# Optimization experiments

Hardware: AMD Instinct MI355X
Metric: run time of the kernel (lower is better)

## Reference

```python
import jax, jax.numpy as jnp
import numpy as np

B, IMG, TXT, DIM, H, D = 1, 1024, 256, 1536, 24, 64
SCALE = 1.0  # control cross-attn scale


def _lin(x, w, b):
    return x @ w + b


def _heads(x):  # [B,S,DIM] -> [B,H,S,D]
    return jnp.swapaxes(x.reshape(x.shape[0], x.shape[1], H, D), 1, 2)


def _merge(x):  # [B,H,S,D] -> [B,S,DIM]
    return jnp.swapaxes(x, 1, 2).reshape(x.shape[0], x.shape[2], H * D)


def _sdpa(q, k, v):
    s = jnp.einsum('bhqd,bhkd->bhqk', q, k) * (1.0 / np.sqrt(D))
    return jnp.einsum('bhqk,bhkd->bhqd', jax.nn.softmax(s, axis=-1), v)


def _rope(x, pe):  # x: [B,H,S,D], pe: [1,1,S,D//2,2,2]
    xr = x.reshape(*x.shape[:-1], -1, 1, 2)  # [B,H,S,D/2,1,2]
    out = pe[..., 0] * xr[..., 0] + pe[..., 1] * xr[..., 1]  # [B,H,S,D/2,2]
    return out.reshape(x.shape)


def _forward(hidden_states, encoder_hidden_states, hidden_states_control,
             encoder_hidden_states_control, img_to_q_control, pe,
             a_q_w, a_q_b, a_k_w, a_k_b, a_v_w, a_v_b,
             a_addq_w, a_addq_b, a_addk_w, a_addk_b, a_addv_w, a_addv_b,
             a_out_w, a_out_b, a_addout_w, a_addout_b,
             c_q_w, c_q_b, c_k_w, c_k_b, c_v_w, c_v_b,
             c_addq_w, c_addq_b, c_addk_w, c_addk_b, c_addv_w, c_addv_b,
             c_out_w, c_out_b, c_addout_w, c_addout_b):
    img_len = hidden_states.shape[1]
    # ---- main joint attention stream (no RoPE, per original) ----
    q = jnp.concatenate([_heads(_lin(hidden_states, a_q_w, a_q_b)),
                         _heads(_lin(encoder_hidden_states, a_addq_w, a_addq_b))], axis=2)
    k = jnp.concatenate([_heads(_lin(hidden_states, a_k_w, a_k_b)),
                         _heads(_lin(encoder_hidden_states, a_addk_w, a_addk_b))], axis=2)
    v = jnp.concatenate([_heads(_lin(hidden_states, a_v_w, a_v_b)),
                         _heads(_lin(encoder_hidden_states, a_addv_w, a_addv_b))], axis=2)
    hs = _merge(_sdpa(q, k, v))
    hs, ehs = hs[:, :img_len], hs[:, img_len:]
    # ---- control joint attention stream (with RoPE) ----
    qc = jnp.concatenate([_heads(_lin(hidden_states_control, c_q_w, c_q_b)),
                          _heads(_lin(encoder_hidden_states_control, c_addq_w, c_addq_b))], axis=2)
    kc = jnp.concatenate([_heads(_lin(hidden_states_control, c_k_w, c_k_b)),
                          _heads(_lin(encoder_hidden_states_control, c_addk_w, c_addk_b))], axis=2)
    vc = jnp.concatenate([_heads(_lin(hidden_states_control, c_v_w, c_v_b)),
                          _heads(_lin(encoder_hidden_states_control, c_addv_w, c_addv_b))], axis=2)
    key_cross, value_cross = kc, vc  # saved BEFORE RoPE, per original
    hsc = _merge(_sdpa(_rope(qc, pe), _rope(kc, pe), vc))
    hsc, ehsc = hsc[:, :img_len], hsc[:, img_len:]
    # ---- cross attention: img query attends to control K/V ----
    q_cross = _rope(_heads(img_to_q_control), pe[:, :, :img_len])
    k_cross = _rope(key_cross, pe[:, :, :key_cross.shape[2]])
    cross = _merge(_sdpa(q_cross, k_cross, value_cross))
    hs = hs + SCALE * cross
    # ---- output projections (to_out[1] is dropout p=0 -> identity) ----
    hs = _lin(hs, a_out_w, a_out_b)
    ehs = _lin(ehs, a_addout_w, a_addout_b)
    hsc = _lin(hsc, c_out_w, c_out_b)
    ehsc = _lin(ehsc, c_addout_w, c_addout_b)
    return hs, ehs, hsc, ehsc


def setup_inputs() -> dict:
    key = jax.random.key(0)
    ki = iter(jax.random.split(key, 80))
    d = {}
    d['hidden_states'] = jax.random.normal(next(ki), (B, IMG, DIM), jnp.float32)
    d['encoder_hidden_states'] = jax.random.normal(next(ki), (B, TXT, DIM), jnp.float32)
    d['hidden_states_control'] = jax.random.normal(next(ki), (B, IMG, DIM), jnp.float32)
    d['encoder_hidden_states_control'] = jax.random.normal(next(ki), (B, TXT, DIM), jnp.float32)
    d['img_to_q_control'] = jax.random.normal(next(ki), (B, IMG, DIM), jnp.float32)
    # realistic rotary pe: [1,1,S,D/2,2,2] rotation matrices
    S = IMG + TXT
    pos = np.arange(S, dtype=np.float32)
    freqs = 1.0 / (10000.0 ** (np.arange(0, D, 2, dtype=np.float32) / D))  # [D/2]
    ang = pos[:, None] * freqs[None, :]  # [S, D/2]
    cos, sin = np.cos(ang), np.sin(ang)
    pe = np.stack([np.stack([cos, -sin], -1), np.stack([sin, cos], -1)], -2)  # [S,D/2,2,2]
    d['pe'] = jnp.asarray(pe)[None, None]
    for p in ('a', 'c'):
        for name in ('q', 'k', 'v', 'addq', 'addk', 'addv', 'out', 'addout'):
            d[f'{p}_{name}_w'] = jax.random.normal(next(ki), (DIM, DIM), jnp.float32) * 0.02
            d[f'{p}_{name}_b'] = jax.random.normal(next(ki), (DIM,), jnp.float32) * 0.01
    return d


def reference(hidden_states, encoder_hidden_states, hidden_states_control,
              encoder_hidden_states_control, img_to_q_control, pe,
              a_q_w, a_q_b, a_k_w, a_k_b, a_v_w, a_v_b,
              a_addq_w, a_addq_b, a_addk_w, a_addk_b, a_addv_w, a_addv_b,
              a_out_w, a_out_b, a_addout_w, a_addout_b,
              c_q_w, c_q_b, c_k_w, c_k_b, c_v_w, c_v_b,
              c_addq_w, c_addq_b, c_addk_w, c_addk_b, c_addv_w, c_addv_b,
              c_out_w, c_out_b, c_addout_w, c_addout_b):
    return _forward(hidden_states, encoder_hidden_states, hidden_states_control,
                    encoder_hidden_states_control, img_to_q_control, pe,
                    a_q_w, a_q_b, a_k_w, a_k_b, a_v_w, a_v_b,
                    a_addq_w, a_addq_b, a_addk_w, a_addk_b, a_addv_w, a_addv_b,
                    a_out_w, a_out_b, a_addout_w, a_addout_b,
                    c_q_w, c_q_b, c_k_w, c_k_b, c_v_w, c_v_b,
                    c_addq_w, c_addq_b, c_addk_w, c_addk_b, c_addv_w, c_addv_b,
                    c_out_w, c_out_b, c_addout_w, c_addout_b)
```

## Files before the change

kernel.cpp:

```cpp
#include <hip/hip_runtime.h>

#define DIM 1536
#define IMG 1024
#define TXT 256
#define SEQ 1280
#define NH 24
#define HD 64
#define SD ((size_t)SEQ * DIM)
#define IDSZ ((size_t)IMG * DIM)
#define WSZ ((size_t)DIM * DIM)

typedef __attribute__((ext_vector_type(8))) short short8;
typedef __attribute__((ext_vector_type(4))) float f32x4;

__device__ __forceinline__ float bf2f(ushort u) {
    union { unsigned int i; float f; } v; v.i = ((unsigned int)u) << 16; return v.f;
}
__device__ __forceinline__ ushort f2bf(float f) {
    union { unsigned int i; float f; } v; v.f = f;
    unsigned int u = v.i;
    u += 0x7fffu + ((u >> 16) & 1u);
    return (ushort)(u >> 16);
}
__device__ __forceinline__ ushort f2bf_rz(float f) {
    union { unsigned int i; float f; } v; v.f = f;
    return (ushort)(v.i >> 16);
}

__global__ __launch_bounds__(256) void detect_dtype(const void* __restrict__ p,
                                                    int* __restrict__ flag)
{
    __shared__ int cnt;
    if (threadIdx.x == 0) cnt = 0;
    __syncthreads();
    const ushort* u = (const ushort*)p;
    int local = 0;
    for (int i = threadIdx.x; i < 2048; i += 256) {
        ushort v = u[2 * i];
        int e = (v >> 7) & 0xFF;
        if (e >= 0xC0) local++;
    }
    atomicAdd(&cnt, local);
    __syncthreads();
    if (threadIdx.x == 0) flag[0] = (cnt > 16) ? 1 : 0;
}

struct CvtP {
    const void* src[20];
    ushort* dst[20];
    int n8[20];
};

__global__ __launch_bounds__(256) void convert_bf16(CvtP p, const int* __restrict__ dflag)
{
    const int a = blockIdx.y;
    const int i = blockIdx.x * 256 + threadIdx.x;
    if (i >= p.n8[a]) return;
    const size_t off = (size_t)i * 8;
    uint4 o;
    if (dflag[0]) {
        const float* s = (const float*)p.src[a] + off;
        const float4 f0 = *(const float4*)s;
        const float4 f1 = *(const float4*)(s + 4);
        ushort t[8];
        t[0] = f2bf(f0.x); t[1] = f2bf(f0.y); t[2] = f2bf(f0.z); t[3] = f2bf(f0.w);
        t[4] = f2bf(f1.x); t[5] = f2bf(f1.y); t[6] = f2bf(f1.z); t[7] = f2bf(f1.w);
        o = *(uint4*)t;
    } else {
        o = *(const uint4*)((const ushort*)p.src[a] + off);
    }
    *(uint4*)(p.dst[a] + off) = o;
}

#define LSTR 40

struct QKV3P {
    const ushort* Xb;
    const ushort* Wb;
    const void* B[12];
    float* Y[6];
    ushort* Yh[6];
    ushort* Yl[6];
};

__global__ __launch_bounds__(256) void gemm_qkv_v4(QKV3P p, const int* __restrict__ dflag)
{
    __shared__ __align__(16) ushort As[2][128 * LSTR];
    __shared__ __align__(16) ushort Bs[2][64 * 64];
    const int dt = dflag[0];
    const int bx = blockIdx.x;
    const int wsel = bx / 12;
    const int n0 = (bx - wsel * 12) * 128;
    const int ys = blockIdx.y;
    const int str = (ys >= 10) ? 1 : 0;
    const int m0g = (ys - str * 10) * 128;
    const bool istxt = (m0g >= IMG);
    const int widx = str * 6 + wsel + (istxt ? 3 : 0);
    const ushort* X  = p.Xb + (size_t)str * SD;
    const ushort* Wp = p.Wb + (size_t)widx * WSZ;
    const void* Bp = p.B[widx];
    const int yidx = str * 3 + wsel;
    float*  Y  = p.Y[yidx];
    ushort* yh = p.Yh[yidx];
    ushort* yl = p.Yl[yidx];

    const int t = threadIdx.x;
    const int wave = t >> 6, lane = t & 63;
    const int quad = lane >> 4, l16 = lane & 15;
    const int wm = (wave >> 1) * 64, wn = (wave & 1) * 64;

    const int arow = t >> 1, apair = t & 1;
    const int bn8 = (t & 15) << 3, bkk = (t >> 4) << 1;
    const int aps = apair ^ ((arow >> 3) & 1);
    const int adst = arow * LSTR + aps * 16;
    const int bkg = bkk >> 3, bo = bkk & 7;

    f32x4 acc[4][4];
#pragma unroll
    for (int i = 0; i < 4; ++i)
#pragma unroll
        for (int j = 0; j < 4; ++j) acc[i][j] = (f32x4)(0.0f);

    uint4 rau[2];
    uint4 rbu[2];

    auto loadA = [&](int k0) {
        const ushort* xp = X + (size_t)(m0g + arow) * DIM + k0 + apair * 16;
        rau[0] = *(const uint4*)xp;
        rau[1] = *(const uint4*)(xp + 8);
    };
    auto loadB = [&](int k0) {
        const ushort* wp0 = Wp + (size_t)(k0 + bkk) * DIM + n0 + bn8;
        rbu[0] = *(const uint4*)wp0;
        rbu[1] = *(const uint4*)(wp0 + DIM);
    };
    auto storeA = [&](int buf) {
        *(uint4*)&As[buf][adst]     = rau[0];
        *(uint4*)&As[buf][adst + 8] = rau[1];
    };
    auto storeB = [&](int buf) {
        ushort t0[8], t1[8];
        *(uint4*)t0 = rbu[0];
        *(uint4*)t1 = rbu[1];
#pragma unroll
        for (int j = 0; j < 8; ++j) {
            const int rr = bn8 + j;
            const int R = rr & 63, half = rr >> 6;
            const int gx = (((half << 2) + bkg) ^ (R & 7) ^ (R >> 3)) & 7;
            *(unsigned int*)&Bs[buf][R * 64 + gx * 8 + bo] =
                (unsigned int)t0[j] | ((unsigned int)t1[j] << 16);
        }
    };

    loadA(0); loadB(0);
    storeA(0); storeB(0);
    __syncthreads();

    for (int k = 0; k < DIM / 32; ++k) {
        const int cur = k & 1;
        const bool hn = (k + 1) < DIM / 32;
        if (hn) { loadA((k + 1) * 32); loadB((k + 1) * 32); }

        short8 b[4];
#pragma unroll
        for (int j = 0; j < 4; ++j) {
            const int rrn = wn + j * 16 + l16;
            const int R = rrn & 63, half = rrn >> 6;
            const int gx = (((half << 2) + quad) ^ (R & 7) ^ (R >> 3)) & 7;
            b[j] = *(const short8*)&Bs[cur][R * 64 + gx * 8];
        }
#pragma unroll
        for (int i = 0; i < 4; ++i) {
            const int rr = wm + i * 16 + l16;
            const int ps = (quad >> 1) ^ ((rr >> 3) & 1);
            const int col = ps * 16 + (quad & 1) * 8;
            short8 a = *(const short8*)&As[cur][rr * LSTR + col];
#pragma unroll
            for (int j = 0; j < 4; ++j)
                acc[i][j] = __builtin_amdgcn_mfma_f32_16x16x32_bf16(a, b[j], acc[i][j], 0, 0, 0);
        }
        if (hn) { storeA(cur ^ 1); storeB(cur ^ 1); }
        __syncthreads();
    }

#pragma unroll
    for (int j = 0; j < 4; ++j) {
        const int col = n0 + wn + j * 16 + l16;
        const float bv = dt ? ((const float*)Bp)[col] : bf2f(((const ushort*)Bp)[col]);
#pragma unroll
        for (int i = 0; i < 4; ++i)
#pragma unroll
            for (int r = 0; r < 4; ++r) {
                const int row = m0g + wm + i * 16 + quad * 4 + r;
                const size_t o = (size_t)row * DIM + col;
                const float val = acc[i][j][r] + bv;
                if (Y) Y[o] = val;
                if (yh) {
                    const ushort hv = f2bf(val);
                    yh[o] = hv;
                    yl[o] = f2bf(val - bf2f(hv));
                }
            }
    }
}

struct OutP {
    const ushort* Xh; const ushort* Xl;
    const ushort* Wb;
    const void* B[4];
    void* out;
};

__global__ __launch_bounds__(256) void gemm_out_v4(OutP p, const int* __restrict__ dflag)
{
    __shared__ __align__(16) ushort Ah[2][64 * LSTR];
    __shared__ __align__(16) ushort Al[2][64 * LSTR];
    __shared__ __align__(16) ushort Bs[2][64 * 64];
    const int dt = dflag[0];
    const int n0 = blockIdx.x * 128;
    const int mt = blockIdx.y;
    const int seg = (mt < 16) ? 0 : (mt < 20) ? 1 : (mt < 36) ? 2 : 3;
    const ushort* Wp = p.Wb + (size_t)seg * WSZ;
    const void* Bp = p.B[seg];
    const int m0 = mt * 64;

    const int t = threadIdx.x;
    const int wave = t >> 6, lane = t & 63;
    const int quad = lane >> 4, l16 = lane & 15;
    const int wm = (wave >> 1) * 32, wn = (wave & 1) * 64;

    const int arow = t >> 2, ag = t & 3;
    const int apg = ag >> 1, asub = ag & 1;
    const int aps = apg ^ ((arow >> 3) & 1);
    const int adst = arow * LSTR + aps * 16 + asub * 8;
    const int bn8 = (t & 15) << 3, bkk = (t >> 4) << 1;
    const int bkg = bkk >> 3, bo = bkk & 7;

    f32x4 acc[2][4];
#pragma unroll
    for (int i = 0; i < 2; ++i)
#pragma unroll
        for (int j = 0; j < 4; ++j) acc[i][j] = (f32x4)(0.0f);

    uint4 rah, ral;
    uint4 rbu[2];

    auto loadA = [&](int k0) {
        const size_t off = (size_t)(m0 + arow) * DIM + k0 + ag * 8;
        rah = *(const uint4*)(p.Xh + off);
        ral = *(const uint4*)(p.Xl + off);
    };
    auto loadB = [&](int k0) {
        const ushort* wp0 = Wp + (size_t)(k0 + bkk) * DIM + n0 + bn8;
        rbu[0] = *(const uint4*)wp0;
        rbu[1] = *(const uint4*)(wp0 + DIM);
    };
    auto storeA = [&](int buf) {
        *(uint4*)&Ah[buf][adst] = rah;
        *(uint4*)&Al[buf][adst] = ral;
    };
    auto storeB = [&](int buf) {
        ushort t0[8], t1[8];
        *(uint4*)t0 = rbu[0];
        *(uint4*)t1 = rbu[1];
#pragma unroll
        for (int j = 0; j < 8; ++j) {
            const int rr = bn8 + j;
            const int R = rr & 63, half = rr >> 6;
            const int gx = (((half << 2) + bkg) ^ (R & 7) ^ (R >> 3)) & 7;
            *(unsigned int*)&Bs[buf][R * 64 + gx * 8 + bo] =
                (unsigned int)t0[j] | ((unsigned int)t1[j] << 16);
        }
    };

    loadA(0); loadB(0);
    storeA(0); storeB(0);
    __syncthreads();

    for (int k = 0; k < DIM / 32; ++k) {
        const int cur = k & 1;
        const bool hn = (k + 1) < DIM / 32;
        if (hn) { loadA((k + 1) * 32); loadB((k + 1) * 32); }

        short8 b[4];
#pragma unroll
        for (int j = 0; j < 4; ++j) {
            const int rrn = wn + j * 16 + l16;
            const int R = rrn & 63, half = rrn >> 6;
            const int gx = (((half << 2) + quad) ^ (R & 7) ^ (R >> 3)) & 7;
            b[j] = *(const short8*)&Bs[cur][R * 64 + gx * 8];
        }
#pragma unroll
        for (int i = 0; i < 2; ++i) {
            const int rr = wm + i * 16 + l16;
            const int ps = (quad >> 1) ^ ((rr >> 3) & 1);
            const int col = ps * 16 + (quad & 1) * 8;
            short8 ah = *(const short8*)&Ah[cur][rr * LSTR + col];
            short8 al = *(const short8*)&Al[cur][rr * LSTR + col];
#pragma unroll
            for (int j = 0; j < 4; ++j) {
                acc[i][j] = __builtin_amdgcn_mfma_f32_16x16x32_bf16(ah, b[j], acc[i][j], 0, 0, 0);
                acc[i][j] = __builtin_amdgcn_mfma_f32_16x16x32_bf16(al, b[j], acc[i][j], 0, 0, 0);
            }
        }
        if (hn) { storeA(cur ^ 1); storeB(cur ^ 1); }
        __syncthreads();
    }

#pragma unroll
    for (int j = 0; j < 4; ++j) {
        const int col = n0 + wn + j * 16 + l16;
        const float bv = dt ? ((const float*)Bp)[col] : bf2f(((const ushort*)Bp)[col]);
#pragma unroll
        for (int i = 0; i < 2; ++i)
#pragma unroll
            for (int r = 0; r < 4; ++r) {
                const int grow = m0 + wm + i * 16 + quad * 4 + r;
                const size_t o = (size_t)grow * DIM + col;
                const float val = acc[i][j][r] + bv;
                if (dt) ((float*)p.out)[o] = val;
                else    ((ushort*)p.out)[o] = f2bf(val);
            }
    }
}

__device__ __forceinline__ void pe_load(const void* pe, int dt, size_t off,
                                        float& c00, float& c01, float& c10, float& c11)
{
    if (dt) {
        float4 pv = *(const float4*)((const float*)pe + off);
        c00 = pv.x; c01 = pv.y; c10 = pv.z; c11 = pv.w;
    } else {
        const ushort* pp = (const ushort*)pe + off;
        c00 = bf2f(pp[0]); c01 = bf2f(pp[1]); c10 = bf2f(pp[2]); c11 = bf2f(pp[3]);
    }
}

struct PrepP {
    const float* v1; const float* vC;
    ushort *vthA, *vtlA, *vthC, *vtlC;
    float* q1;
    const float* k1; ushort *khC, *kloC;
    const void* i2q; float* qx;
    const void* pe;
};

#define VT_BLKS 960
#define RN0 (SEQ * 768)
#define RN1 (SEQ * 768)
#define RN2 (IMG * 768)

__global__ __launch_bounds__(256) void prep_fused(PrepP p, const int* __restrict__ dflag)
{
    __shared__ unsigned int tile[64 * 65];
    const int dt = dflag[0];
    const int bx = blockIdx.x;
    const int t = threadIdx.x;

    if (bx < VT_BLKS) {
        const int z = bx / 480, rem = bx - z * 480;
        const int s0 = (rem % 20) * 64, h = rem / 20;
        const float* V = z ? p.vC : p.v1;
        ushort* Vth = z ? p.vthC : p.vthA;
        ushort* Vtl = z ? p.vtlC : p.vtlA;
#pragma unroll
        for (int it = 0; it < 16; ++it) {
            const int sl = (t >> 6) + (it << 2);
            const int d = t & 63;
            const float v = V[(size_t)(s0 + sl) * DIM + h * HD + d];
            const ushort hv = f2bf(v);
            const ushort lv = f2bf(v - bf2f(hv));
            tile[d * 65 + sl] = (unsigned int)hv | ((unsigned int)lv << 16);
        }
        __syncthreads();
        const int d = t >> 2, cc = (t & 3) << 4;
        ushort th[16], tl[16];
#pragma unroll
        for (int j = 0; j < 16; ++j) {
            const unsigned int w = tile[d * 65 + cc + j];
            th[j] = (ushort)w;
            tl[j] = (ushort)(w >> 16);
        }
        const size_t off = (size_t)(h * HD + d) * SEQ + s0 + cc;
        *(uint4*)(Vth + off)     = *(uint4*)&th[0];
        *(uint4*)(Vth + off + 8) = *(uint4*)&th[8];
        *(uint4*)(Vtl + off)     = *(uint4*)&tl[0];
        *(uint4*)(Vtl + off + 8) = *(uint4*)&tl[8];
        return;
    }

    int idx = (bx - VT_BLKS) * 256 + t;
    if (idx < RN0) {
        int s = idx / 768, pp = idx - s * 768;
        int col = pp << 1, i = pp & 31;
        float* bp = p.q1 + (size_t)s * DIM + col;
        float x0 = bp[0], x1 = bp[1];
        float c00, c01, c10, c11;
        pe_load(p.pe, dt, (size_t)s * 128 + i * 4, c00, c01, c10, c11);
        bp[0] = c00 * x0 + c01 * x1;
        bp[1] = c10 * x0 + c11 * x1;
        return;
    }
    idx -= RN0;
    if (idx < RN1) {
        int s = idx / 768, pp = idx - s * 768;
        int col = pp << 1, i = pp & 31;
        float2 xv = *(const float2*)(p.k1 + (size_t)s * DIM + col);
        float c00, c01, c10, c11;
        pe_load(p.pe, dt, (size_t)s * 128 + i * 4, c00, c01, c10, c11);
        float y0 = c00 * xv.x + c01 * xv.y;
        float y1 = c10 * xv.x + c11 * xv.y;
        ushort h0 = f2bf(y0), h1 = f2bf(y1);
        ushort l0 = f2bf(y0 - bf2f(h0)), l1 = f2bf(y1 - bf2f(h1));
        *(unsigned int*)(p.khC  + (size_t)s * DIM + col) = (unsigned int)h0 | ((unsigned int)h1 << 16);
        *(unsigned int*)(p.kloC + (size_t)s * DIM + col) = (unsigned int)l0 | ((unsigned int)l1 << 16);
        return;
    }
    idx -= RN1;
    if (idx < RN2) {
        int s = idx / 768, pp = idx - s * 768;
        int col = pp << 1, i = pp & 31;
        float x0, x1;
        if (dt) {
            float2 xv = *(const float2*)((const float*)p.i2q + (size_t)s * DIM + col);
            x0 = xv.x; x1 = xv.y;
        } else {
            const ushort* sp = (const ushort*)p.i2q + (size_t)s * DIM + col;
            x0 = bf2f(sp[0]); x1 = bf2f(sp[1]);
        }
        float c00, c01, c10, c11;
        pe_load(p.pe, dt, (size_t)s * 128 + i * 4, c00, c01, c10, c11);
        float* dp = p.qx + (size_t)s * DIM + col;
        dp[0] = c00 * x0 + c01 * x1;
        dp[1] = c10 * x0 + c11 * x1;
    }
}

__device__ __forceinline__ int swz(int row, int col) {
    return row * 64 + ((((col >> 3) ^ row) & 7) << 3) + (col & 7);
}
__device__ __forceinline__ short8 ldfrag(const ushort* plane, int row, int col) {
    return *(const short8*)&plane[swz(row, col)];
}

struct AttnAllP {
    const float* Qf[3];
    const ushort* Kh[3]; const ushort* Kl[3];
    const ushort* Vth[3]; const ushort* Vtl[3];
    float* Op0[3]; float* Op1[3];
    float2* Ml[3];
    int mlq[3];
};

__global__ __launch_bounds__(256) void attn_all(AttnAllP p)
{
    __shared__ ushort Qh_[4096], Ql_[4096];
    __shared__ ushort Kh_[4096], Kl_[4096];
    __shared__ ushort Vh_[4096], Vl_[4096];

    const int bx = blockIdx.x;
    const int seg = (bx < 20) ? 0 : (bx < 40) ? 1 : 2;
    const int q0 = (bx - ((seg == 0) ? 0 : (seg == 1) ? 20 : 40)) * 64;
    const int h = blockIdx.y;
    const int z = blockIdx.z;
    const int t = threadIdx.x;
    const int wave = t >> 6, lane = t & 63;
    const int quad = lane >> 4, l16 = lane & 15;
    const int wq0 = wave * 16;

    const float* Qf = p.Qf[seg];
    const ushort* Kh = p.Kh[seg]; const ushort* Kl = p.Kl[seg];
    const ushort* Vth = p.Vth[seg]; const ushort* Vtl = p.Vtl[seg];

    const int srow = t >> 2, c0 = (t & 3) << 4;
    const int g0 = c0 >> 3;
    const int p0 = ((g0 ^ (srow & 7)) & 7) << 3;
    const int p1 = (((g0 + 1) ^ (srow & 7)) & 7) << 3;

    {
        const float* src = Qf + (size_t)(q0 + srow) * DIM + h * HD + c0;
        float x[16];
        *(float4*)&x[0]  = *(const float4*)(src);
        *(float4*)&x[4]  = *(const float4*)(src + 4);
        *(float4*)&x[8]  = *(const float4*)(src + 8);
        *(float4*)&x[12] = *(const float4*)(src + 12);
        ushort hi[16], lo[16];
#pragma unroll
        for (int i = 0; i < 16; ++i) {
            const float xs = x[i] * 0.125f;
            hi[i] = f2bf(xs);
            lo[i] = f2bf(xs - bf2f(hi[i]));
        }
        *(uint4*)&Qh_[srow * 64 + p0] = *(uint4*)&hi[0];
        *(uint4*)&Qh_[srow * 64 + p1] = *(uint4*)&hi[8];
        *(uint4*)&Ql_[srow * 64 + p0] = *(uint4*)&lo[0];
        *(uint4*)&Ql_[srow * 64 + p1] = *(uint4*)&lo[8];
    }
    short8 qfh[2], qfl[2];
#pragma unroll
    for (int c = 0; c < 2; ++c) {
        qfh[c] = ldfrag(Qh_, wq0 + l16, c * 32 + quad * 8);
        qfl[c] = ldfrag(Ql_, wq0 + l16, c * 32 + quad * 8);
    }

    float m_[4], l_[4];
#pragma unroll
    for (int r = 0; r < 4; ++r) { m_[r] = -3e38f; l_[r] = 0.0f; }
    f32x4 Oacc[4];
#pragma unroll
    for (int j = 0; j < 4; ++j) Oacc[j] = (f32x4)(0.0f);

    const int kvbeg = z * (SEQ / 2);
    for (int kt = 0; kt < SEQ / 2; kt += 64) {
        const int kv0 = kvbeg + kt;
        __syncthreads();
        {
            const size_t off = (size_t)(kv0 + srow) * DIM + h * HD + c0;
            *(uint4*)&Kh_[srow * 64 + p0] = *(const uint4*)(Kh + off);
            *(uint4*)&Kh_[srow * 64 + p1] = *(const uint4*)(Kh + off + 8);
            *(uint4*)&Kl_[srow * 64 + p0] = *(const uint4*)(Kl + off);
            *(uint4*)&Kl_[srow * 64 + p1] = *(const uint4*)(Kl + off + 8);
        }
        {
            const size_t off = (size_t)(h * HD + srow) * SEQ + kv0 + c0;
            *(uint4*)&Vh_[srow * 64 + p0] = *(const uint4*)(Vth + off);
            *(uint4*)&Vh_[srow * 64 + p1] = *(const uint4*)(Vth + off + 8);
            *(uint4*)&Vl_[srow * 64 + p0] = *(const uint4*)(Vtl + off);
            *(uint4*)&Vl_[srow * 64 + p1] = *(const uint4*)(Vtl + off + 8);
        }
        __syncthreads();

        f32x4 S[4];
#pragma unroll
        for (int j = 0; j < 4; ++j) S[j] = (f32x4)(0.0f);
        __builtin_amdgcn_s_setprio(1);
#pragma unroll
        for (int c = 0; c < 2; ++c) {
#pragma unroll
            for (int j = 0; j < 4; ++j) {
                short8 bh = ldfrag(Kh_, j * 16 + l16, c * 32 + quad * 8);
                short8 bl = ldfrag(Kl_, j * 16 + l16, c * 32 + quad * 8);
                S[j] = __builtin_amdgcn_mfma_f32_16x16x32_bf16(qfh[c], bh, S[j], 0, 0, 0);
                S[j] = __builtin_amdgcn_mfma_f32_16x16x32_bf16(qfl[c], bh, S[j], 0, 0, 0);
                S[j] = __builtin_amdgcn_mfma_f32_16x16x32_bf16(qfh[c], bl, S[j], 0, 0, 0);
            }
        }
        __builtin_amdgcn_s_setprio(0);

        float alpha[4];
#pragma unroll
        for (int r = 0; r < 4; ++r) {
            float mx = fmaxf(fmaxf(S[0][r], S[1][r]), fmaxf(S[2][r], S[3][r]));
            mx = fmaxf(mx, __shfl_xor(mx, 1));
            mx = fmaxf(mx, __shfl_xor(mx, 2));
            mx = fmaxf(mx, __shfl_xor(mx, 4));
            mx = fmaxf(mx, __shfl_xor(mx, 8));
            float mn = fmaxf(m_[r], mx);
            alpha[r] = __expf(m_[r] - mn);
            m_[r] = mn;
            float rs = 0.0f;
#pragma unroll
            for (int j = 0; j < 4; ++j) {
                float pv = __expf(S[j][r] - mn);
                S[j][r] = pv;
                rs += pv;
            }
            rs += __shfl_xor(rs, 1);
            rs += __shfl_xor(rs, 2);
            rs += __shfl_xor(rs, 4);
            rs += __shfl_xor(rs, 8);
            l_[r] = l_[r] * alpha[r] + rs;
        }
#pragma unroll
        for (int j = 0; j < 4; ++j)
#pragma unroll
            for (int r = 0; r < 4; ++r) Oacc[j][r] *= alpha[r];

        {
            const int prow = wq0 + quad * 4;
#pragma unroll
            for (int j = 0; j < 4; ++j)
#pragma unroll
                for (int r = 0; r < 4; ++r) {
                    float pv = S[j][r];
                    ushort ph = f2bf(pv);
                    ushort pl = f2bf_rz(pv - bf2f(ph));
                    int idx = swz(prow + r, j * 16 + l16);
                    Qh_[idx] = ph;
                    Ql_[idx] = pl;
                }
        }

        __builtin_amdgcn_s_setprio(1);
#pragma unroll
        for (int c = 0; c < 2; ++c) {
            short8 pah = ldfrag(Qh_, wq0 + l16, c * 32 + quad * 8);
            short8 pal = ldfrag(Ql_, wq0 + l16, c * 32 + quad * 8);
#pragma unroll
            for (int jn = 0; jn < 4; ++jn) {
                short8 vbh = ldfrag(Vh_, jn * 16 + l16, c * 32 + quad * 8);
                short8 vbl = ldfrag(Vl_, jn * 16 + l16, c * 32 + quad * 8);
                Oacc[jn] = __builtin_amdgcn_mfma_f32_16x16x32_bf16(pah, vbh, Oacc[jn], 0, 0, 0);
                Oacc[jn] = __builtin_amdgcn_mfma_f32_16x16x32_bf16(pal, vbh, Oacc[jn], 0, 0, 0);
                Oacc[jn] = __builtin_amdgcn_mfma_f32_16x16x32_bf16(pah, vbl, Oacc[jn], 0, 0, 0);
            }
        }
        __builtin_amdgcn_s_setprio(0);
    }

    float* Opz = z ? p.Op1[seg] : p.Op0[seg];
    const int mlq = p.mlq[seg];
    float2* Ml = p.Ml[seg];
#pragma unroll
    for (int r = 0; r < 4; ++r) {
        const int rowq = q0 + wq0 + quad * 4 + r;
        if (l16 == 0)
            Ml[((size_t)z * NH + h) * mlq + rowq] = make_float2(m_[r], l_[r]);
#pragma unroll
        for (int jn = 0; jn < 4; ++jn)
            Opz[(size_t)rowq * DIM + h * HD + jn * 16 + l16] = Oacc[jn][r];
    }
}

struct MergeP {
    const float *pA0, *pA1, *pC0, *pC1, *pX0, *pX1;
    const float2 *MlA, *MlC, *MlX;
    ushort *Xh, *Xl;
};

__device__ __forceinline__ float4 comb2(const float* O0, const float* O1,
                                        const float2* Ml, int mlq, int row, int c4)
{
    const int h = c4 >> 6;
    const float2 a = Ml[(size_t)h * mlq + row];
    const float2 b = Ml[(size_t)(NH + h) * mlq + row];
    const float ms = fmaxf(a.x, b.x);
    const float s0 = __expf(a.x - ms), s1 = __expf(b.x - ms);
    const float inv = 1.0f / (s0 * a.y + s1 * b.y);
    const float4 o0 = *(const float4*)&O0[(size_t)row * DIM + c4];
    const float4 o1 = *(const float4*)&O1[(size_t)row * DIM + c4];
    float4 r;
    r.x = (s0 * o0.x + s1 * o1.x) * inv;
    r.y = (s0 * o0.y + s1 * o1.y) * inv;
    r.z = (s0 * o0.z + s1 * o1.z) * inv;
    r.w = (s0 * o0.w + s1 * o1.w) * inv;
    return r;
}

__global__ __launch_bounds__(256) void merge_all(MergeP p)
{
    const int idx = blockIdx.x * 256 + threadIdx.x;
    if (idx >= 2560 * 384) return;
    const int row = idx / 384;
    const int c4 = (idx - row * 384) << 2;
    float4 r;
    if (row < SEQ) {
        r = comb2(p.pA0, p.pA1, p.MlA, SEQ, row, c4);
        if (row < IMG) {
            const float4 x = comb2(p.pX0, p.pX1, p.MlX, IMG, row, c4);
            r.x += x.x; r.y += x.y; r.z += x.z; r.w += x.w;
        }
    } else {
        r = comb2(p.pC0, p.pC1, p.MlC, SEQ, row - SEQ, c4);
    }
    float v[4] = {r.x, r.y, r.z, r.w};
    ushort hi[4], lo[4];
#pragma unroll
    for (int j = 0; j < 4; ++j) {
        hi[j] = f2bf(v[j]);
        lo[j] = f2bf(v[j] - bf2f(hi[j]));
    }
    const size_t o = (size_t)row * DIM + c4;
    *(uint2*)(p.Xh + o) = *(uint2*)hi;
    *(uint2*)(p.Xl + o) = *(uint2*)lo;
}

extern "C" void kernel_launch(void* const* d_in, const int* in_sizes, int n_in,
                              void* d_out, int out_size, void* d_ws, size_t ws_size,
                              hipStream_t stream) {
    (void)in_sizes; (void)n_in; (void)out_size; (void)ws_size;
    const void* hs   = d_in[0];
    const void* ehs  = d_in[1];
    const void* hsc  = d_in[2];
    const void* ehsc = d_in[3];
    const void* i2q  = d_in[4];
    const void* pe   = d_in[5];
#define W_(i) ((const void*)d_in[i])

    char* base = (char*)d_ws;
    int* flag = (int*)base;
    char* ptr = base + 256;
    auto alloc = [&](size_t bytes) { char* r = ptr; ptr += bytes; return r; };
    float* q1  = (float*)alloc(SD * 4);
    float* k1  = (float*)alloc(SD * 4);
    float* v1  = (float*)alloc(SD * 4);
    float* vC  = (float*)alloc(SD * 4);
    float* qA  = (float*)alloc(SD * 4);
    float* qx  = (float*)alloc(IDSZ * 4);
    ushort* khA  = (ushort*)alloc(SD * 2);
    ushort* kloA = (ushort*)alloc(SD * 2);
    ushort* vthA = (ushort*)alloc(SD * 2);
    ushort* vtlA = (ushort*)alloc(SD * 2);
    ushort* khC  = (ushort*)alloc(SD * 2);
    ushort* kloC = (ushort*)alloc(SD * 2);
    ushort* vthC = (ushort*)alloc(SD * 2);
    ushort* vtlC = (ushort*)alloc(SD * 2);
    float* pX0 = (float*)alloc(IDSZ * 4);
    float* pX1 = (float*)alloc(IDSZ * 4);
    float2* MlA = (float2*)alloc((size_t)2 * NH * SEQ * 8);
    float2* MlC = (float2*)alloc((size_t)2 * NH * SEQ * 8);
    float2* MlX = (float2*)alloc((size_t)2 * NH * IMG * 8);
    ushort* Wbf = (ushort*)alloc(16 * WSZ * 2);
    ushort* Xbf = (ushort*)alloc(2 * SD * 2);
    float* pC1 = (float*)Xbf;
    ushort* Xh = (ushort*)qA;
    ushort* Xl = (ushort*)q1;

    dim3 blk(256);
    detect_dtype<<<1, blk, 0, stream>>>(hs, flag);

    {
        CvtP cp;
        const int wsrc[16] = {6, 8, 10, 12, 14, 16, 22, 24, 26, 28, 30, 32,
                              18, 20, 34, 36};
        for (int j = 0; j < 16; ++j) {
            cp.src[j] = W_(wsrc[j]);
            cp.dst[j] = Wbf + (size_t)j * WSZ;
            cp.n8[j] = (int)(WSZ / 8);
        }
        cp.src[16] = hs;   cp.dst[16] = Xbf;             cp.n8[16] = (int)(IDSZ / 8);
        cp.src[17] = ehs;  cp.dst[17] = Xbf + IDSZ;      cp.n8[17] = (int)((size_t)TXT * DIM / 8);
        cp.src[18] = hsc;  cp.dst[18] = Xbf + SD;        cp.n8[18] = (int)(IDSZ / 8);
        cp.src[19] = ehsc; cp.dst[19] = Xbf + SD + IDSZ; cp.n8[19] = (int)((size_t)TXT * DIM / 8);
        convert_bf16<<<dim3((int)(WSZ / 8 + 255) / 256, 20), blk, 0, stream>>>(cp, flag);
    }

    QKV3P qp;
    qp.Xb = Xbf;
    qp.Wb = Wbf;
    {
        const int bsrc[12] = {7, 9, 11, 13, 15, 17, 23, 25, 27, 29, 31, 33};
        for (int j = 0; j < 12; ++j) qp.B[j] = W_(bsrc[j]);
    }
    for (int j = 0; j < 6; ++j) { qp.Y[j] = nullptr; qp.Yh[j] = nullptr; qp.Yl[j] = nullptr; }
    qp.Y[0] = qA;
    qp.Yh[1] = khA; qp.Yl[1] = kloA;
    qp.Y[2] = v1;
    qp.Y[3] = q1;
    qp.Y[4] = k1;
    qp.Y[5] = vC;
    gemm_qkv_v4<<<dim3(36, 20), blk, 0, stream>>>(qp, flag);

    {
        PrepP pp;
        pp.v1 = v1; pp.vC = vC;
        pp.vthA = vthA; pp.vtlA = vtlA; pp.vthC = vthC; pp.vtlC = vtlC;
        pp.q1 = q1;
        pp.k1 = k1; pp.khC = khC; pp.kloC = kloC;
        pp.i2q = i2q; pp.qx = qx;
        pp.pe = pe;
        const int ropeBlocks = (RN0 + RN1 + RN2 + 255) / 256;
        prep_fused<<<VT_BLKS + ropeBlocks, blk, 0, stream>>>(pp, flag);
    }

    {
        AttnAllP ap;
        ap.Qf[0] = qA; ap.Qf[1] = q1; ap.Qf[2] = qx;
        ap.Kh[0] = khA; ap.Kl[0] = kloA;
        ap.Kh[1] = khC; ap.Kl[1] = kloC;
        ap.Kh[2] = khC; ap.Kl[2] = kloC;
        ap.Vth[0] = vthA; ap.Vtl[0] = vtlA;
        ap.Vth[1] = vthC; ap.Vtl[1] = vtlC;
        ap.Vth[2] = vthC; ap.Vtl[2] = vtlC;
        ap.Op0[0] = v1;  ap.Op1[0] = k1;
        ap.Op0[1] = vC;  ap.Op1[1] = pC1;
        ap.Op0[2] = pX0; ap.Op1[2] = pX1;
        ap.Ml[0] = MlA; ap.Ml[1] = MlC; ap.Ml[2] = MlX;
        ap.mlq[0] = SEQ; ap.mlq[1] = SEQ; ap.mlq[2] = IMG;
        attn_all<<<dim3(56, NH, 2), blk, 0, stream>>>(ap);
    }

    {
        MergeP mp;
        mp.pA0 = v1; mp.pA1 = k1;
        mp.pC0 = vC; mp.pC1 = pC1;
        mp.pX0 = pX0; mp.pX1 = pX1;
        mp.MlA = MlA; mp.MlC = MlC; mp.MlX = MlX;
        mp.Xh = Xh; mp.Xl = Xl;
        merge_all<<<(2560 * 384 + 255) / 256, blk, 0, stream>>>(mp);
    }

    {
        OutP op;
        op.Xh = Xh; op.Xl = Xl;
        op.Wb = Wbf + (size_t)12 * WSZ;
        op.B[0] = W_(19); op.B[1] = W_(21); op.B[2] = W_(35); op.B[3] = W_(37);
        op.out = d_out;
        gemm_out_v4<<<dim3(12, 40), blk, 0, stream>>>(op, flag);
    }
#undef W_
}
```

Baseline: 552.2 us.

## Pre-swizzle weights into tiled LDS image and drop Q shared buffers in attention

Weight conversion now writes each 32x128 weight tile already laid out in the swizzled LDS format. The QKV and output GEMMs can then load B tiles with contiguous 16-byte loads and store them to LDS with two vector stores, instead of eight scattered 32-bit stores per thread. Separately, the attention kernel reuses the K shared buffers for Q and P staging, which removes the Qh/Ql arrays to cut LDS use and may raise occupancy. This adds a __syncthreads before P is written. The weight conversion kernel is split from the activation conversion.

```diff
diff --git a/kernel.cpp b/kernel.cpp
--- a/kernel.cpp
+++ b/kernel.cpp
@@ -9,6 +9,9 @@
 #define SD ((size_t)SEQ * DIM)
 #define IDSZ ((size_t)IMG * DIM)
 #define WSZ ((size_t)DIM * DIM)
+#define NTIL 12
+#define KTIL 48
+#define TILE_USH 4096
 
 typedef __attribute__((ext_vector_type(8))) short short8;
 typedef __attribute__((ext_vector_type(4))) float f32x4;
@@ -46,9 +49,9 @@
 }
 
 struct CvtP {
-    const void* src[20];
-    ushort* dst[20];
-    int n8[20];
+    const void* src[4];
+    ushort* dst[4];
+    int n8[4];
 };
 
 __global__ __launch_bounds__(256) void convert_bf16(CvtP p, const int* __restrict__ dflag)
@@ -72,32 +75,76 @@
     *(uint4*)(p.dst[a] + off) = o;
 }
 
+struct WImgP {
+    const void* src[16];
+    ushort* img;
+};
+
+__global__ __launch_bounds__(256) void convert_wimg(WImgP p, const int* __restrict__ dflag)
+{
+    const int widx = blockIdx.y;
+    const int nt = blockIdx.x / KTIL, kt = blockIdx.x - nt * KTIL;
+    const int t = threadIdx.x;
+    const int bn8 = (t & 15) << 3, bkk = (t >> 4) << 1;
+    const int bkg = bkk >> 3, bo = bkk & 7;
+    const int k0 = kt * 32, n0 = nt * 128;
+
+    ushort t0[8], t1[8];
+    if (dflag[0]) {
+        const float* w = (const float*)p.src[widx];
+        const float* r0 = w + (size_t)(k0 + bkk) * DIM + n0 + bn8;
+        float x0[8], x1[8];
+        *(float4*)&x0[0] = *(const float4*)r0;
+        *(float4*)&x0[4] = *(const float4*)(r0 + 4);
+        *(float4*)&x1[0] = *(const float4*)(r0 + DIM);
+        *(float4*)&x1[4] = *(const float4*)(r0 + DIM + 4);
+#pragma unroll
+        for (int j = 0; j < 8; ++j) { t0[j] = f2bf(x0[j]); t1[j] = f2bf(x1[j]); }
+    } else {
+        const ushort* w = (const ushort*)p.src[widx];
+        const ushort* r0 = w + (size_t)(k0 + bkk) * DIM + n0 + bn8;
+        *(uint4*)t0 = *(const uint4*)r0;
+        *(uint4*)t1 = *(const uint4*)(r0 + DIM);
+    }
+
+    ushort* img = p.img + (((size_t)widx * NTIL + nt) * KTIL + kt) * TILE_USH;
+#pragma unroll
+    for (int j = 0; j < 8; ++j) {
+        const int rr = bn8 + j;
+        const int R = rr & 63, half = rr >> 6;
+        const int gx = (((half << 2) + bkg) ^ (R & 7) ^ (R >> 3)) & 7;
+        *(unsigned int*)&img[R * 64 + gx * 8 + bo] =
+            (unsigned int)t0[j] | ((unsigned int)t1[j] << 16);
+    }
+}
+
 #define LSTR 40
 
 struct QKV3P {
     const ushort* Xb;
-    const ushort* Wb;
+    const ushort* Wimg;
     const void* B[12];
     float* Y[6];
     ushort* Yh[6];
     ushort* Yl[6];
 };
 
-__global__ __launch_bounds__(256) void gemm_qkv_v4(QKV3P p, const int* __restrict__ dflag)
+__global__ __launch_bounds__(256) void gemm_qkv_v5(QKV3P p, const int* __restrict__ dflag)
 {
     __shared__ __align__(16) ushort As[2][128 * LSTR];
     __shared__ __align__(16) ushort Bs[2][64 * 64];
     const int dt = dflag[0];
     const int bx = blockIdx.x;
     const int wsel = bx / 12;
-    const int n0 = (bx - wsel * 12) * 128;
+    const int nt = bx - wsel * 12;
+    const int n0 = nt * 128;
     const int ys = blockIdx.y;
     const int str = (ys >= 10) ? 1 : 0;
     const int m0g = (ys - str * 10) * 128;
     const bool istxt = (m0g >= IMG);
     const int widx = str * 6 + wsel + (istxt ? 3 : 0);
     const ushort* X  = p.Xb + (size_t)str * SD;
-    const ushort* Wp = p.Wb + (size_t)widx * WSZ;
+    const ushort* img0 = p.Wimg + (((size_t)widx * NTIL + nt) * KTIL) * TILE_USH;
     const void* Bp = p.B[widx];
     const int yidx = str * 3 + wsel;
     float*  Y  = p.Y[yidx];
@@ -110,10 +157,8 @@
     const int wm = (wave >> 1) * 64, wn = (wave & 1) * 64;
 
     const int arow = t >> 1, apair = t & 1;
-    const int bn8 = (t & 15) << 3, bkk = (t >> 4) << 1;
     const int aps = apair ^ ((arow >> 3) & 1);
     const int adst = arow * LSTR + aps * 16;
-    const int bkg = bkk >> 3, bo = bkk & 7;
 
     f32x4 acc[4][4];
 #pragma unroll
@@ -130,26 +175,17 @@
         rau[1] = *(const uint4*)(xp + 8);
     };
     auto loadB = [&](int k0) {
-        const ushort* wp0 = Wp + (size_t)(k0 + bkk) * DIM + n0 + bn8;
-        rbu[0] = *(const uint4*)wp0;
-        rbu[1] = *(const uint4*)(wp0 + DIM);
+        const ushort* ip = img0 + (size_t)(k0 >> 5) * TILE_USH + t * 8;
+        rbu[0] = *(const uint4*)ip;
+        rbu[1] = *(const uint4*)(ip + 2048);
     };
     auto storeA = [&](int buf) {
         *(uint4*)&As[buf][adst]     = rau[0];
         *(uint4*)&As[buf][adst + 8] = rau[1];
     };
     auto storeB = [&](int buf) {
-        ushort t0[8], t1[8];
-        *(uint4*)t0 = rbu[0];
-        *(uint4*)t1 = rbu[1];
-#pragma unroll
-        for (int j = 0; j < 8; ++j) {
-            const int rr = bn8 + j;
-            const int R = rr & 63, half = rr >> 6;
-            const int gx = (((half << 2) + bkg) ^ (R & 7) ^ (R >> 3)) & 7;
-            *(unsigned int*)&Bs[buf][R * 64 + gx * 8 + bo] =
-                (unsigned int)t0[j] | ((unsigned int)t1[j] << 16);
-        }
+        *(uint4*)&Bs[buf][t * 8]        = rbu[0];
+        *(uint4*)&Bs[buf][2048 + t * 8] = rbu[1];
     };
 
     loadA(0); loadB(0);
@@ -206,21 +242,22 @@
 
 struct OutP {
     const ushort* Xh; const ushort* Xl;
-    const ushort* Wb;
+    const ushort* Wimg;
     const void* B[4];
     void* out;
 };
 
-__global__ __launch_bounds__(256) void gemm_out_v4(OutP p, const int* __restrict__ dflag)
+__global__ __launch_bounds__(256) void gemm_out_v5(OutP p, const int* __restrict__ dflag)
 {
     __shared__ __align__(16) ushort Ah[2][64 * LSTR];
     __shared__ __align__(16) ushort Al[2][64 * LSTR];
     __shared__ __align__(16) ushort Bs[2][64 * 64];
     const int dt = dflag[0];
-    const int n0 = blockIdx.x * 128;
+    const int nt = blockIdx.x;
+    const int n0 = nt * 128;
     const int mt = blockIdx.y;
     const int seg = (mt < 16) ? 0 : (mt < 20) ? 1 : (mt < 36) ? 2 : 3;
-    const ushort* Wp = p.Wb + (size_t)seg * WSZ;
+    const ushort* img0 = p.Wimg + (((size_t)(12 + seg) * NTIL + nt) * KTIL) * TILE_USH;
     const void* Bp = p.B[seg];
     const int m0 = mt * 64;
 
@@ -233,8 +270,6 @@
     const int apg = ag >> 1, asub = ag & 1;
     const int aps = apg ^ ((arow >> 3) & 1);
     const int adst = arow * LSTR + aps * 16 + asub * 8;
-    const int bn8 = (t & 15) << 3, bkk = (t >> 4) << 1;
-    const int bkg = bkk >> 3, bo = bkk & 7;
 
     f32x4 acc[2][4];
 #pragma unroll
@@ -251,26 +286,17 @@
         ral = *(const uint4*)(p.Xl + off);
     };
     auto loadB = [&](int k0) {
-        const ushort* wp0 = Wp + (size_t)(k0 + bkk) * DIM + n0 + bn8;
-        rbu[0] = *(const uint4*)wp0;
-        rbu[1] = *(const uint4*)(wp0 + DIM);
+        const ushort* ip = img0 + (size_t)(k0 >> 5) * TILE_USH + t * 8;
+        rbu[0] = *(const uint4*)ip;
+        rbu[1] = *(const uint4*)(ip + 2048);
     };
     auto storeA = [&](int buf) {
         *(uint4*)&Ah[buf][adst] = rah;
         *(uint4*)&Al[buf][adst] = ral;
     };
     auto storeB = [&](int buf) {
-        ushort t0[8], t1[8];
-        *(uint4*)t0 = rbu[0];
-        *(uint4*)t1 = rbu[1];
-#pragma unroll
-        for (int j = 0; j < 8; ++j) {
-            const int rr = bn8 + j;
-            const int R = rr & 63, half = rr >> 6;
-            const int gx = (((half << 2) + bkg) ^ (R & 7) ^ (R >> 3)) & 7;
-            *(unsigned int*)&Bs[buf][R * 64 + gx * 8 + bo] =
-                (unsigned int)t0[j] | ((unsigned int)t1[j] << 16);
-        }
+        *(uint4*)&Bs[buf][t * 8]        = rbu[0];
+        *(uint4*)&Bs[buf][2048 + t * 8] = rbu[1];
     };
 
     loadA(0); loadB(0);
@@ -454,7 +480,6 @@
 
 __global__ __launch_bounds__(256) void attn_all(AttnAllP p)
 {
-    __shared__ ushort Qh_[4096], Ql_[4096];
     __shared__ ushort Kh_[4096], Kl_[4096];
     __shared__ ushort Vh_[4096], Vl_[4096];
 
@@ -491,16 +516,16 @@
             hi[i] = f2bf(xs);
             lo[i] = f2bf(xs - bf2f(hi[i]));
         }
-        *(uint4*)&Qh_[srow * 64 + p0] = *(uint4*)&hi[0];
-        *(uint4*)&Qh_[srow * 64 + p1] = *(uint4*)&hi[8];
-        *(uint4*)&Ql_[srow * 64 + p0] = *(uint4*)&lo[0];
-        *(uint4*)&Ql_[srow * 64 + p1] = *(uint4*)&lo[8];
+        *(uint4*)&Kh_[srow * 64 + p0] = *(uint4*)&hi[0];
+        *(uint4*)&Kh_[srow * 64 + p1] = *(uint4*)&hi[8];
+        *(uint4*)&Kl_[srow * 64 + p0] = *(uint4*)&lo[0];
+        *(uint4*)&Kl_[srow * 64 + p1] = *(uint4*)&lo[8];
     }
     short8 qfh[2], qfl[2];
 #pragma unroll
     for (int c = 0; c < 2; ++c) {
-        qfh[c] = ldfrag(Qh_, wq0 + l16, c * 32 + quad * 8);
-        qfl[c] = ldfrag(Ql_, wq0 + l16, c * 32 + quad * 8);
+        qfh[c] = ldfrag(Kh_, wq0 + l16, c * 32 + quad * 8);
+        qfl[c] = ldfrag(Kl_, wq0 + l16, c * 32 + quad * 8);
     }
 
     float m_[4], l_[4];
@@ -576,6 +601,8 @@
 #pragma unroll
             for (int r = 0; r < 4; ++r) Oacc[j][r] *= alpha[r];
 
+        __syncthreads();
+
         {
             const int prow = wq0 + quad * 4;
 #pragma unroll
@@ -586,16 +613,16 @@
                     ushort ph = f2bf(pv);
                     ushort pl = f2bf_rz(pv - bf2f(ph));
                     int idx = swz(prow + r, j * 16 + l16);
-                    Qh_[idx] = ph;
-                    Ql_[idx] = pl;
+                    Kh_[idx] = ph;
+                    Kl_[idx] = pl;
                 }
         }
 
         __builtin_amdgcn_s_setprio(1);
 #pragma unroll
         for (int c = 0; c < 2; ++c) {
-            short8 pah = ldfrag(Qh_, wq0 + l16, c * 32 + quad * 8);
-            short8 pal = ldfrag(Ql_, wq0 + l16, c * 32 + quad * 8);
+            short8 pah = ldfrag(Kh_, wq0 + l16, c * 32 + quad * 8);
+            short8 pal = ldfrag(Kl_, wq0 + l16, c * 32 + quad * 8);
 #pragma unroll
             for (int jn = 0; jn < 4; ++jn) {
                 short8 vbh = ldfrag(Vh_, jn * 16 + l16, c * 32 + quad * 8);
@@ -710,7 +737,7 @@
     float2* MlA = (float2*)alloc((size_t)2 * NH * SEQ * 8);
     float2* MlC = (float2*)alloc((size_t)2 * NH * SEQ * 8);
     float2* MlX = (float2*)alloc((size_t)2 * NH * IMG * 8);
-    ushort* Wbf = (ushort*)alloc(16 * WSZ * 2);
+    ushort* Wimg = (ushort*)alloc((size_t)16 * NTIL * KTIL * TILE_USH * 2);
     ushort* Xbf = (ushort*)alloc(2 * SD * 2);
     float* pC1 = (float*)Xbf;
     ushort* Xh = (ushort*)qA;
@@ -720,24 +747,24 @@
     detect_dtype<<<1, blk, 0, stream>>>(hs, flag);
 
     {
-        CvtP cp;
+        WImgP wp;
         const int wsrc[16] = {6, 8, 10, 12, 14, 16, 22, 24, 26, 28, 30, 32,
                               18, 20, 34, 36};
-        for (int j = 0; j < 16; ++j) {
-            cp.src[j] = W_(wsrc[j]);
-            cp.dst[j] = Wbf + (size_t)j * WSZ;
-            cp.n8[j] = (int)(WSZ / 8);
-        }
-        cp.src[16] = hs;   cp.dst[16] = Xbf;             cp.n8[16] = (int)(IDSZ / 8);
-        cp.src[17] = ehs;  cp.dst[17] = Xbf + IDSZ;      cp.n8[17] = (int)((size_t)TXT * DIM / 8);
-        cp.src[18] = hsc;  cp.dst[18] = Xbf + SD;        cp.n8[18] = (int)(IDSZ / 8);
-        cp.src[19] = ehsc; cp.dst[19] = Xbf + SD + IDSZ; cp.n8[19] = (int)((size_t)TXT * DIM / 8);
-        convert_bf16<<<dim3((int)(WSZ / 8 + 255) / 256, 20), blk, 0, stream>>>(cp, flag);
+        for (int j = 0; j < 16; ++j) wp.src[j] = W_(wsrc[j]);
+        wp.img = Wimg;
+        convert_wimg<<<dim3(NTIL * KTIL, 16), blk, 0, stream>>>(wp, flag);
+
+        CvtP cp;
+        cp.src[0] = hs;   cp.dst[0] = Xbf;             cp.n8[0] = (int)(IDSZ / 8);
+        cp.src[1] = ehs;  cp.dst[1] = Xbf + IDSZ;      cp.n8[1] = (int)((size_t)TXT * DIM / 8);
+        cp.src[2] = hsc;  cp.dst[2] = Xbf + SD;        cp.n8[2] = (int)(IDSZ / 8);
+        cp.src[3] = ehsc; cp.dst[3] = Xbf + SD + IDSZ; cp.n8[3] = (int)((size_t)TXT * DIM / 8);
+        convert_bf16<<<dim3((int)(IDSZ / 8 + 255) / 256, 4), blk, 0, stream>>>(cp, flag);
     }
 
     QKV3P qp;
     qp.Xb = Xbf;
-    qp.Wb = Wbf;
+    qp.Wimg = Wimg;
     {
         const int bsrc[12] = {7, 9, 11, 13, 15, 17, 23, 25, 27, 29, 31, 33};
         for (int j = 0; j < 12; ++j) qp.B[j] = W_(bsrc[j]);
@@ -749,7 +776,7 @@
     qp.Y[3] = q1;
     qp.Y[4] = k1;
     qp.Y[5] = vC;
-    gemm_qkv_v4<<<dim3(36, 20), blk, 0, stream>>>(qp, flag);
+    gemm_qkv_v5<<<dim3(36, 20), blk, 0, stream>>>(qp, flag);
 
     {
         PrepP pp;
@@ -793,10 +820,10 @@
     {
         OutP op;
         op.Xh = Xh; op.Xl = Xl;
-        op.Wb = Wbf + (size_t)12 * WSZ;
+        op.Wimg = Wimg;
         op.B[0] = W_(19); op.B[1] = W_(21); op.B[2] = W_(35); op.B[3] = W_(37);
         op.out = d_out;
-        gemm_out_v4<<<dim3(12, 40), blk, 0, stream>>>(op, flag);
+        gemm_out_v5<<<dim3(12, 40), blk, 0, stream>>>(op, flag);
     }
 #undef W_
 }
```

Measured after the change: 611.2 us. 10.7% more time.

## Drop split-KV in attention and normalize output in-kernel

Applied to the files above, without the earlier changes.

Each attention block now processes the whole KV sequence instead of half, and applies the 1/l normalization in its epilogue. The merge kernel no longer combines two partials with log-sum-exp stats; it only adds the streams and splits into bf16 hi/lo. This removes writing and reading the partial outputs and stats buffers, at the cost of half as many attention blocks, each running a loop twice as long, which may reduce latency hiding and GPU fill.

```diff
diff --git a/kernel.cpp b/kernel.cpp
--- a/kernel.cpp
+++ b/kernel.cpp
@@ -447,9 +447,7 @@
     const float* Qf[3];
     const ushort* Kh[3]; const ushort* Kl[3];
     const ushort* Vth[3]; const ushort* Vtl[3];
-    float* Op0[3]; float* Op1[3];
-    float2* Ml[3];
-    int mlq[3];
+    float* O[3];
 };
 
 __global__ __launch_bounds__(256) void attn_all(AttnAllP p)
@@ -462,7 +460,6 @@
     const int seg = (bx < 20) ? 0 : (bx < 40) ? 1 : 2;
     const int q0 = (bx - ((seg == 0) ? 0 : (seg == 1) ? 20 : 40)) * 64;
     const int h = blockIdx.y;
-    const int z = blockIdx.z;
     const int t = threadIdx.x;
     const int wave = t >> 6, lane = t & 63;
     const int quad = lane >> 4, l16 = lane & 15;
@@ -510,9 +507,7 @@
 #pragma unroll
     for (int j = 0; j < 4; ++j) Oacc[j] = (f32x4)(0.0f);
 
-    const int kvbeg = z * (SEQ / 2);
-    for (int kt = 0; kt < SEQ / 2; kt += 64) {
-        const int kv0 = kvbeg + kt;
+    for (int kv0 = 0; kv0 < SEQ; kv0 += 64) {
         __syncthreads();
         {
             const size_t off = (size_t)(kv0 + srow) * DIM + h * HD + c0;
@@ -608,46 +603,25 @@
         __builtin_amdgcn_s_setprio(0);
     }
 
-    float* Opz = z ? p.Op1[seg] : p.Op0[seg];
-    const int mlq = p.mlq[seg];
-    float2* Ml = p.Ml[seg];
+    float* O = p.O[seg];
+    float inv[4];
+#pragma unroll
+    for (int r = 0; r < 4; ++r) inv[r] = 1.0f / l_[r];
 #pragma unroll
     for (int r = 0; r < 4; ++r) {
         const int rowq = q0 + wq0 + quad * 4 + r;
-        if (l16 == 0)
-            Ml[((size_t)z * NH + h) * mlq + rowq] = make_float2(m_[r], l_[r]);
 #pragma unroll
         for (int jn = 0; jn < 4; ++jn)
-            Opz[(size_t)rowq * DIM + h * HD + jn * 16 + l16] = Oacc[jn][r];
+            O[(size_t)rowq * DIM + h * HD + jn * 16 + l16] = Oacc[jn][r] * inv[r];
     }
 }
 
 struct MergeP {
-    const float *pA0, *pA1, *pC0, *pC1, *pX0, *pX1;
-    const float2 *MlA, *MlC, *MlX;
+    const float *oA, *oC, *oX;
     ushort *Xh, *Xl;
 };
 
-__device__ __forceinline__ float4 comb2(const float* O0, const float* O1,
-                                        const float2* Ml, int mlq, int row, int c4)
-{
-    const int h = c4 >> 6;
-    const float2 a = Ml[(size_t)h * mlq + row];
-    const float2 b = Ml[(size_t)(NH + h) * mlq + row];
-    const float ms = fmaxf(a.x, b.x);
-    const float s0 = __expf(a.x - ms), s1 = __expf(b.x - ms);
-    const float inv = 1.0f / (s0 * a.y + s1 * b.y);
-    const float4 o0 = *(const float4*)&O0[(size_t)row * DIM + c4];
-    const float4 o1 = *(const float4*)&O1[(size_t)row * DIM + c4];
-    float4 r;
-    r.x = (s0 * o0.x + s1 * o1.x) * inv;
-    r.y = (s0 * o0.y + s1 * o1.y) * inv;
-    r.z = (s0 * o0.z + s1 * o1.z) * inv;
-    r.w = (s0 * o0.w + s1 * o1.w) * inv;
-    return r;
-}
-
-__global__ __launch_bounds__(256) void merge_all(MergeP p)
+__global__ __launch_bounds__(256) void merge_lite(MergeP p)
 {
     const int idx = blockIdx.x * 256 + threadIdx.x;
     if (idx >= 2560 * 384) return;
@@ -655,13 +629,13 @@
     const int c4 = (idx - row * 384) << 2;
     float4 r;
     if (row < SEQ) {
-        r = comb2(p.pA0, p.pA1, p.MlA, SEQ, row, c4);
+        r = *(const float4*)&p.oA[(size_t)row * DIM + c4];
         if (row < IMG) {
-            const float4 x = comb2(p.pX0, p.pX1, p.MlX, IMG, row, c4);
+            const float4 x = *(const float4*)&p.oX[(size_t)row * DIM + c4];
             r.x += x.x; r.y += x.y; r.z += x.z; r.w += x.w;
         }
     } else {
-        r = comb2(p.pC0, p.pC1, p.MlC, SEQ, row - SEQ, c4);
+        r = *(const float4*)&p.oC[(size_t)(row - SEQ) * DIM + c4];
     }
     float v[4] = {r.x, r.y, r.z, r.w};
     ushort hi[4], lo[4];
@@ -705,14 +679,8 @@
     ushort* kloC = (ushort*)alloc(SD * 2);
     ushort* vthC = (ushort*)alloc(SD * 2);
     ushort* vtlC = (ushort*)alloc(SD * 2);
-    float* pX0 = (float*)alloc(IDSZ * 4);
-    float* pX1 = (float*)alloc(IDSZ * 4);
-    float2* MlA = (float2*)alloc((size_t)2 * NH * SEQ * 8);
-    float2* MlC = (float2*)alloc((size_t)2 * NH * SEQ * 8);
-    float2* MlX = (float2*)alloc((size_t)2 * NH * IMG * 8);
     ushort* Wbf = (ushort*)alloc(16 * WSZ * 2);
     ushort* Xbf = (ushort*)alloc(2 * SD * 2);
-    float* pC1 = (float*)Xbf;
     ushort* Xh = (ushort*)qA;
     ushort* Xl = (ushort*)q1;
 
@@ -772,22 +740,17 @@
         ap.Vth[0] = vthA; ap.Vtl[0] = vtlA;
         ap.Vth[1] = vthC; ap.Vtl[1] = vtlC;
         ap.Vth[2] = vthC; ap.Vtl[2] = vtlC;
-        ap.Op0[0] = v1;  ap.Op1[0] = k1;
-        ap.Op0[1] = vC;  ap.Op1[1] = pC1;
-        ap.Op0[2] = pX0; ap.Op1[2] = pX1;
-        ap.Ml[0] = MlA; ap.Ml[1] = MlC; ap.Ml[2] = MlX;
-        ap.mlq[0] = SEQ; ap.mlq[1] = SEQ; ap.mlq[2] = IMG;
-        attn_all<<<dim3(56, NH, 2), blk, 0, stream>>>(ap);
+        ap.O[0] = v1;
+        ap.O[1] = vC;
+        ap.O[2] = k1;
+        attn_all<<<dim3(56, NH), blk, 0, stream>>>(ap);
     }
 
     {
         MergeP mp;
-        mp.pA0 = v1; mp.pA1 = k1;
-        mp.pC0 = vC; mp.pC1 = pC1;
-        mp.pX0 = pX0; mp.pX1 = pX1;
-        mp.MlA = MlA; mp.MlC = MlC; mp.MlX = MlX;
+        mp.oA = v1; mp.oC = vC; mp.oX = k1;
         mp.Xh = Xh; mp.Xl = Xl;
-        merge_all<<<(2560 * 384 + 255) / 256, blk, 0, stream>>>(mp);
+        merge_lite<<<(2560 * 384 + 255) / 256, blk, 0, stream>>>(mp);
     }
 
     {
```

New measurement: 555.6 us. Within noise of the previous version (+0.6%).
